# Optimization experiments

Hardware: AMD Instinct MI355X
Metric: run time of the kernel (lower is better)

The kernel has to match this reference:

```python
import jax, jax.numpy as jnp
import numpy as np

# Grid constants from voxel_size=(0.2,0.2,4), point_cloud_range=(0,-40,-3,70.4,40,1)
VX, VY, VZ = 0.2, 0.2, 4.0
PCR = (0.0, -40.0, -3.0, 70.4, 40.0, 1.0)
NX, NY, NZ = 352, 400, 1   # round((hi-lo)/v) per axis
BATCH = 2
N_POINTS = 400000
CANVAS = BATCH * NZ * NY * NX  # dense canvas of all voxels (segment ids)
EPS = 1e-3  # BN1d eps from norm_cfg


def _vidx(coors):
    # linear voxel index: b*Z*Y*X + z*Y*X + y*X + x  (coors = [b,z,y,x])
    c = coors.astype(jnp.int32)
    return ((c[:, 0] * NZ + c[:, 1]) * NY + c[:, 2]) * NX + c[:, 3]


def _seg_mean(x, idx):
    # scatter-mean over voxels (DynamicScatter, average_points=True)
    s = jax.ops.segment_sum(x, idx, num_segments=CANVAS)
    c = jax.ops.segment_sum(jnp.ones((x.shape[0], 1), x.dtype), idx, num_segments=CANVAS)
    return s / jnp.maximum(c, 1.0)


def _seg_max(x, idx):
    # scatter-max over voxels (DynamicScatter, average_points=False); empty voxels -> 0
    m = jax.ops.segment_max(x, idx, num_segments=CANVAS)
    c = jax.ops.segment_sum(jnp.ones((x.shape[0],), x.dtype), idx, num_segments=CANVAS)
    return jnp.where((c > 0)[:, None], m, jnp.zeros_like(m))


def _bn_relu(x, g, b):
    # BN1d in training mode (batch stats, biased var), affine, then ReLU
    mu = x.mean(axis=0)
    var = x.var(axis=0)
    return jax.nn.relu((x - mu) * jax.lax.rsqrt(var + EPS) * g + b)


def setup_inputs() -> dict:
    key = jax.random.key(0)
    ks = jax.random.split(key, 6)
    features = jax.random.normal(ks[0], (N_POINTS, 4), jnp.float32)
    # coors [b, z, y, x]; batch column sorted so coors[-1,0]+1 == batch_size
    half = N_POINTS // 2
    b = jnp.concatenate([jnp.zeros(half, jnp.int32), jnp.ones(N_POINTS - half, jnp.int32)])
    z = jnp.zeros(N_POINTS, jnp.int32)  # NZ == 1
    y = jax.random.randint(ks[1], (N_POINTS,), 0, NY, jnp.int32)
    x = jax.random.randint(ks[2], (N_POINTS,), 0, NX, jnp.int32)
    coors = jnp.stack([b, z, y, x], axis=1)
    # VFE params: layer0 Linear(10->64, no bias), layer1 Linear(128->128, no bias)
    W0 = jax.random.normal(ks[3], (10, 64), jnp.float32) * 0.1
    g0 = jnp.ones((64,), jnp.float32)
    b0 = jnp.zeros((64,), jnp.float32)
    W1 = jax.random.normal(ks[4], (128, 128), jnp.float32) * 0.1
    g1 = jnp.ones((128,), jnp.float32)
    b1 = jnp.zeros((128,), jnp.float32)
    return {"features": features, "coors": coors, "W0": W0, "g0": g0, "b0": b0,
            "W1": W1, "g1": g1, "b1": b1}


def reference(features, coors, W0, g0, b0, W1, g1, b1):
    idx = _vidx(coors)
    # cluster center: scatter-mean of point features, gather back to points
    vmean = _seg_mean(features, idx)
    pts_mean = vmean[idx]
    f_cluster = features[:, :3] - pts_mean[:, :3]
    # voxel center offset
    cf = coors.astype(features.dtype)
    f_center = jnp.stack([
        features[:, 0] - (cf[:, 3] * VX + (VX / 2 + PCR[0])),
        features[:, 1] - (cf[:, 2] * VY + (VY / 2 + PCR[1])),
        features[:, 2] - (cf[:, 1] * VZ + (VZ / 2 + PCR[2])),
    ], axis=1)
    feat = jnp.concatenate([features, f_cluster, f_center], axis=1)  # (N, 10)
    # VFE layer 0 + voxel max pool + gather-broadcast + concat
    pf0 = _bn_relu(feat @ W0, g0, b0)           # (N, 64)
    v0 = _seg_max(pf0, idx)                     # (CANVAS, 64)
    feat1 = jnp.concatenate([pf0, v0[idx]], axis=1)  # (N, 128)
    # VFE layer 1 + final voxel max pool
    pf1 = _bn_relu(feat1 @ W1, g1, b1)          # (N, 128)
    voxel_feats = _seg_max(pf1, idx)            # (CANVAS, 128), dense canvas
    return voxel_feats
```

## Files before the change

kernel.cpp:

```cpp
#include <hip/hip_runtime.h>

#define NPTS 400000
#define NXv 352
#define NYv 400
#define CANVAS 281600
#define NBLK2 6250
#define SCANB 275

typedef unsigned int uint;
typedef unsigned short ushort;
typedef __attribute__((ext_vector_type(8))) short short8;
typedef __attribute__((ext_vector_type(4))) float floatx4;

__device__ inline uint packbf(float a, float b) {
    uint ua = __float_as_uint(a);
    ua = (ua + 0x7fffu + ((ua >> 16) & 1u)) >> 16;
    uint ub = __float_as_uint(b);
    ub = (ub + 0x7fffu + ((ub >> 16) & 1u)) & 0xffff0000u;
    return ua | ub;
}
__device__ inline ushort bf16bits(float a) {
    uint u = __float_as_uint(a);
    return (ushort)((u + 0x7fffu + ((u >> 16) & 1u)) >> 16);
}
__device__ inline float lo16(uint u) { return __uint_as_float(u << 16); }
__device__ inline float hi16(uint u) { return __uint_as_float(u & 0xffff0000u); }
__device__ inline float bfval(ushort u) { return __uint_as_float(((uint)u) << 16); }

__global__ void k_bucket(const int4* __restrict__ coors, int* __restrict__ idxbuf,
                         int* __restrict__ pidx, uint* __restrict__ ucnt) {
    int i = blockIdx.x * 256 + threadIdx.x;
    if (i >= NPTS) return;
    int4 c = coors[i];
    int idx = ((c.x + c.y) * NYv + c.z) * NXv + c.w;
    idxbuf[i] = idx;
    pidx[i] = (int)atomicAdd(&ucnt[idx], 1u);
}

__global__ __launch_bounds__(1024) void k_scanA(const uint* __restrict__ ucnt,
                                                uint* __restrict__ voff,
                                                uint* __restrict__ bsum) {
    __shared__ uint sh[1024];
    int t = threadIdx.x;
    int v = blockIdx.x * 1024 + t;
    uint val = ucnt[v];
    sh[t] = val;
    for (int off = 1; off < 1024; off <<= 1) {
        __syncthreads();
        uint x = (t >= off) ? sh[t - off] : 0u;
        __syncthreads();
        sh[t] += x;
    }
    uint incl = sh[t];
    voff[v] = incl - val;
    if (t == 1023) bsum[blockIdx.x] = incl;
}

__global__ __launch_bounds__(1024) void k_scanC(const uint* __restrict__ bsum,
                                                uint* __restrict__ voff) {
    __shared__ uint sh[1024];
    __shared__ uint bs[1024];
    int t = threadIdx.x;
    uint val = (t < SCANB) ? bsum[t] : 0u;
    sh[t] = val; bs[t] = val;
    for (int off = 1; off < 1024; off <<= 1) {
        __syncthreads();
        uint x = (t >= off) ? sh[t - off] : 0u;
        __syncthreads();
        sh[t] += x;
    }
    __syncthreads();
    uint off_ = sh[blockIdx.x] - bs[blockIdx.x];
    int v = blockIdx.x * 1024 + t;
    voff[v] += off_;
    if (blockIdx.x == SCANB - 1 && t == 1023) voff[CANVAS] = NPTS;
}

__global__ void k_perm(const int* __restrict__ idxbuf, const int* __restrict__ pidx,
                       const uint* __restrict__ voff, int* __restrict__ perm,
                       int* __restrict__ vidx) {
    int i = blockIdx.x * 256 + threadIdx.x;
    if (i >= NPTS) return;
    int idx = idxbuf[i];
    uint j = voff[idx] + (uint)pidx[i];
    perm[j] = i;
    vidx[j] = idx;
}

__global__ void k_vmean(const float4* __restrict__ feat, const uint* __restrict__ voff,
                        const int* __restrict__ perm, float4* __restrict__ vmean) {
    int v = blockIdx.x * 256 + threadIdx.x;
    if (v >= CANVAS) return;
    uint s_ = voff[v], e_ = voff[v + 1];
    float4 s = make_float4(0.f, 0.f, 0.f, 0.f);
    for (uint j = s_; j < e_; ++j) {
        float4 f = feat[perm[j]];
        s.x += f.x; s.y += f.y; s.z += f.z; s.w += f.w;
    }
    float inv = 1.0f / (float)max((int)(e_ - s_), 1);
    vmean[v] = make_float4(s.x * inv, s.y * inv, s.z * inv, s.w * inv);
}

__global__ void k_prepw(const float* __restrict__ W1, ushort* __restrict__ w1t) {
    int i = blockIdx.x * 256 + threadIdx.x;
    if (i >= 16384) return;
    int n = i & 127, k = i >> 7;
    w1t[n * 128 + k] = bf16bits(W1[k * 128 + n]);
}

__global__ __launch_bounds__(256) void k_gemm1(
        const float4* __restrict__ feat, const int4* __restrict__ coors,
        const int* __restrict__ perm, const int* __restrict__ vidx,
        const float4* __restrict__ vmean, const float* __restrict__ W0,
        uint* __restrict__ x0u, float* __restrict__ stats) {
    __shared__ float w0s[640];
    __shared__ __align__(8) ushort tile[256 * 68];
    __shared__ float ps[128], qs[128];
    for (int t = threadIdx.x; t < 640; t += 256) w0s[t] = W0[t];
    __syncthreads();
    int j = blockIdx.x * 256 + threadIdx.x;
    bool valid = j < NPTS;
    ushort* trow = &tile[threadIdx.x * 68];
    if (valid) {
        int i = perm[j];
        float4 f = feat[i];
        int4 c = coors[i];
        float4 vm = vmean[vidx[j]];
        float ft[10];
        ft[0] = f.x; ft[1] = f.y; ft[2] = f.z; ft[3] = f.w;
        ft[4] = f.x - vm.x;
        ft[5] = f.y - vm.y;
        ft[6] = f.z - vm.z;
        ft[7] = f.x - ((float)c.w * 0.2f + 0.1f);
        ft[8] = f.y - ((float)c.z * 0.2f + (0.1f - 40.0f));
        ft[9] = f.z - ((float)c.y * 4.0f + (2.0f - 3.0f));
        uint* o = x0u + (size_t)j * 32;
        #pragma unroll
        for (int g = 0; g < 8; ++g) {
            float a[8];
            #pragma unroll
            for (int q = 0; q < 8; ++q) a[q] = 0.f;
            #pragma unroll
            for (int k = 0; k < 10; ++k) {
                float fk = ft[k];
                #pragma unroll
                for (int q = 0; q < 8; ++q) a[q] = fmaf(fk, w0s[k * 64 + g * 8 + q], a[q]);
            }
            uint4 w;
            w.x = packbf(a[0], a[1]); w.y = packbf(a[2], a[3]);
            w.z = packbf(a[4], a[5]); w.w = packbf(a[6], a[7]);
            *(uint4*)(o + g * 4) = w;
            ((uint2*)trow)[g * 2 + 0] = make_uint2(w.x, w.y);
            ((uint2*)trow)[g * 2 + 1] = make_uint2(w.z, w.w);
        }
    } else {
        #pragma unroll
        for (int g = 0; g < 16; ++g) ((uint2*)trow)[g] = make_uint2(0u, 0u);
    }
    __syncthreads();
    if (threadIdx.x < 128) {
        int c = threadIdx.x & 63, half = threadIdx.x >> 6;
        float s = 0.f, q = 0.f;
        for (int r = half * 128; r < half * 128 + 128; ++r) {
            float xv = bfval(tile[r * 68 + c]);
            s += xv;
            q = fmaf(xv, xv, q);
        }
        ps[half * 64 + c] = s;
        qs[half * 64 + c] = q;
    }
    __syncthreads();
    if (threadIdx.x < 64) {
        int c = threadIdx.x;
        atomicAdd(&stats[c], ps[c] + ps[64 + c]);
        atomicAdd(&stats[64 + c], qs[c] + qs[64 + c]);
    }
}

__global__ void k_bnfin(const float* __restrict__ sums, const float* __restrict__ g,
                        const float* __restrict__ b, float* __restrict__ ss, int C,
                        float invN) {
    int j = threadIdx.x;
    if (j >= C) return;
    float mu = sums[j] * invN;
    float var = sums[C + j] * invN - mu * mu;
    float istd = 1.0f / sqrtf(var + 1e-3f);
    float scale = istd * g[j];
    ss[j] = scale;
    ss[C + j] = b[j] - mu * scale;
}

__global__ void k_vmax0(const uint* __restrict__ x0u, const uint* __restrict__ voff,
                        const float* __restrict__ ss, uint* __restrict__ v0u) {
    __shared__ float s[128];
    if (threadIdx.x < 128) s[threadIdx.x] = ss[threadIdx.x];
    __syncthreads();
    int t = blockIdx.x * 256 + threadIdx.x;
    int v = t >> 4;
    if (v >= CANVAS) return;
    int c = (t & 15) << 2;
    uint s_ = voff[v], e_ = voff[v + 1];
    float4 m = make_float4(0.f, 0.f, 0.f, 0.f);
    for (uint j = s_; j < e_; ++j) {
        uint2 u = *(const uint2*)(x0u + (size_t)j * 32 + (c >> 1));
        m.x = fmaxf(m.x, fmaf(lo16(u.x), s[c + 0], s[64 + c + 0]));
        m.y = fmaxf(m.y, fmaf(hi16(u.x), s[c + 1], s[64 + c + 1]));
        m.z = fmaxf(m.z, fmaf(lo16(u.y), s[c + 2], s[64 + c + 2]));
        m.w = fmaxf(m.w, fmaf(hi16(u.y), s[c + 3], s[64 + c + 3]));
    }
    uint2 o; o.x = packbf(m.x, m.y); o.y = packbf(m.z, m.w);
    *(uint2*)(v0u + (size_t)v * 32 + (c >> 1)) = o;
}

__global__ __launch_bounds__(256) void k_gemm2m(
        const uint* __restrict__ x0u, const uint* __restrict__ v0u,
        const int* __restrict__ vidx, const float* __restrict__ ss,
        const ushort* __restrict__ w1t, uint* __restrict__ x1u,
        float* __restrict__ partial) {
    __shared__ __align__(16) ushort Bs[128 * 136];
    __shared__ __align__(16) ushort As[64 * 136];
    __shared__ float pst[4096];
    __shared__ float s[128];
    __shared__ int idxs[64];

    int r0 = blockIdx.x * 64;
    for (int i = threadIdx.x; i < 2048; i += 256) {
        int r = i >> 4, ch = i & 15;
        *(uint4*)&Bs[r * 136 + ch * 8] = *(const uint4*)&w1t[r * 128 + ch * 8];
    }
    if (threadIdx.x < 128) s[threadIdx.x] = ss[threadIdx.x];
    if (threadIdx.x < 64) idxs[threadIdx.x] = vidx[r0 + threadIdx.x];
    __syncthreads();

    for (int i = threadIdx.x; i < 512; i += 256) {
        int r = i >> 3, ch = i & 7, cb = ch * 8;
        uint4 u = *(const uint4*)(x0u + (size_t)(r0 + r) * 32 + ch * 4);
        uint w[4] = {u.x, u.y, u.z, u.w}, o[4];
        #pragma unroll
        for (int q2 = 0; q2 < 4; ++q2) {
            float a = fmaxf(fmaf(lo16(w[q2]), s[cb + 2 * q2], s[64 + cb + 2 * q2]), 0.f);
            float b = fmaxf(fmaf(hi16(w[q2]), s[cb + 2 * q2 + 1], s[64 + cb + 2 * q2 + 1]), 0.f);
            o[q2] = packbf(a, b);
        }
        *(uint4*)&As[r * 136 + ch * 8] = make_uint4(o[0], o[1], o[2], o[3]);
    }
    for (int i = threadIdx.x; i < 512; i += 256) {
        int r = i >> 3, ch = i & 7;
        *(uint4*)&As[r * 136 + 64 + ch * 8] =
            *(const uint4*)(v0u + (size_t)idxs[r] * 32 + ch * 4);
    }
    __syncthreads();

    int lane = threadIdx.x & 63, wid = threadIdx.x >> 6;
    int m = lane & 15, q = lane >> 4;
    const ushort* ar = &As[(wid * 16 + m) * 136 + q * 8];
    short8 a0 = *(const short8*)&ar[0];
    short8 a1 = *(const short8*)&ar[32];
    short8 a2 = *(const short8*)&ar[64];
    short8 a3 = *(const short8*)&ar[96];
    __syncthreads();

    #pragma unroll
    for (int ct = 0; ct < 8; ++ct) {
        const ushort* br = &Bs[(ct * 16 + m) * 136 + q * 8];
        short8 b0 = *(const short8*)&br[0];
        short8 b1 = *(const short8*)&br[32];
        short8 b2 = *(const short8*)&br[64];
        short8 b3 = *(const short8*)&br[96];
        floatx4 acc = {0.f, 0.f, 0.f, 0.f};
        acc = __builtin_amdgcn_mfma_f32_16x16x32_bf16(a0, b0, acc, 0, 0, 0);
        acc = __builtin_amdgcn_mfma_f32_16x16x32_bf16(a1, b1, acc, 0, 0, 0);
        acc = __builtin_amdgcn_mfma_f32_16x16x32_bf16(a2, b2, acc, 0, 0, 0);
        acc = __builtin_amdgcn_mfma_f32_16x16x32_bf16(a3, b3, acc, 0, 0, 0);
        float psv = acc[0] + acc[1] + acc[2] + acc[3];
        float pq = acc[0] * acc[0];
        pq = fmaf(acc[1], acc[1], pq);
        pq = fmaf(acc[2], acc[2], pq);
        pq = fmaf(acc[3], acc[3], pq);
        int col = ct * 16 + m;
        pst[(wid * 4 + q) * 128 + col] = psv;
        pst[2048 + (wid * 4 + q) * 128 + col] = pq;
        #pragma unroll
        for (int rg = 0; rg < 4; ++rg)
            As[(wid * 16 + q * 4 + rg) * 136 + ct * 16 + m] = bf16bits(acc[rg]);
    }
    __syncthreads();

    for (int i = threadIdx.x; i < 1024; i += 256) {
        int r = i >> 4, ch = i & 15;
        *(uint4*)(x1u + (size_t)(r0 + r) * 64 + ch * 4) = *(const uint4*)&As[r * 136 + ch * 8];
    }
    {
        int t = threadIdx.x;
        int base = (t < 128) ? 0 : 2048;
        int c = t & 127;
        float acc = 0.f;
        #pragma unroll
        for (int k = 0; k < 16; ++k) acc += pst[base + k * 128 + c];
        partial[(size_t)blockIdx.x * 256 + t] = acc;
    }
}

__global__ void k_red(const float* __restrict__ partial, float* __restrict__ sums) {
    int c = threadIdx.x;
    float s = 0.f;
    for (int r = blockIdx.x; r < NBLK2; r += gridDim.x) s += partial[(size_t)r * 256 + c];
    atomicAdd(&sums[c], s);
}

__global__ void k_vmax1(const uint2* __restrict__ x1u, const uint* __restrict__ voff,
                        const float* __restrict__ ss, float4* __restrict__ out) {
    __shared__ float s[256];
    s[threadIdx.x] = ss[threadIdx.x];
    __syncthreads();
    int t = blockIdx.x * 256 + threadIdx.x;
    int v = t >> 5;
    if (v >= CANVAS) return;
    int c = (t & 31) << 2;
    uint s_ = voff[v], e_ = voff[v + 1];
    float4 m = make_float4(0.f, 0.f, 0.f, 0.f);
    for (uint j = s_; j < e_; ++j) {
        uint2 u = x1u[(size_t)j * 32 + (c >> 2)];
        m.x = fmaxf(m.x, fmaf(lo16(u.x), s[c + 0], s[128 + c + 0]));
        m.y = fmaxf(m.y, fmaf(hi16(u.x), s[c + 1], s[128 + c + 1]));
        m.z = fmaxf(m.z, fmaf(lo16(u.y), s[c + 2], s[128 + c + 2]));
        m.w = fmaxf(m.w, fmaf(hi16(u.y), s[c + 3], s[128 + c + 3]));
    }
    out[(size_t)v * 32 + (c >> 2)] = m;
}

extern "C" void kernel_launch(void* const* d_in, const int* in_sizes, int n_in,
                              void* d_out, int out_size, void* d_ws, size_t ws_size,
                              hipStream_t stream) {
    const float4* feat  = (const float4*)d_in[0];
    const int4*   coors = (const int4*)d_in[1];
    const float*  W0    = (const float*)d_in[2];
    const float*  g0    = (const float*)d_in[3];
    const float*  b0    = (const float*)d_in[4];
    const float*  W1    = (const float*)d_in[5];
    const float*  g1    = (const float*)d_in[6];
    const float*  b1    = (const float*)d_in[7];

    char* ws = (char*)d_ws;
    int*    idxbuf = (int*)(ws + 0);
    int*    pidx   = (int*)(ws + 1600000);
    uint*   ucnt   = (uint*)(ws + 3200000);
    uint*   voff   = (uint*)(ws + 4326400);
    uint*   bsum   = (uint*)(ws + 5452816);
    float*  stats  = (float*)(ws + 5453936);
    int*    perm   = (int*)(ws + 5457008);
    int*    vidx   = (int*)(ws + 7057008);
    float*  vmean  = (float*)(ws + 8657008);
    ushort* w1t    = (ushort*)(ws + 13162608);
    uint*   x0u    = (uint*)(ws + 13195376);
    uint*   v0u    = (uint*)(ws + 64395376);
    uint*   x1u    = (uint*)(ws + 100440176);
    float*  part   = (float*)(ws + 202840176);

    hipMemsetAsync(ucnt, 0, 1126400, stream);
    hipMemsetAsync(stats, 0, 384 * sizeof(float), stream);

    const int BLK = 256;
    int gpts = (NPTS + BLK - 1) / BLK;
    int gvox = (CANVAS + BLK - 1) / BLK;

    k_bucket<<<gpts, BLK, 0, stream>>>(coors, idxbuf, pidx, ucnt);
    k_prepw<<<64, BLK, 0, stream>>>(W1, w1t);
    k_scanA<<<SCANB, 1024, 0, stream>>>(ucnt, voff, bsum);
    k_scanC<<<SCANB, 1024, 0, stream>>>(bsum, voff);
    k_perm<<<gpts, BLK, 0, stream>>>(idxbuf, pidx, voff, perm, vidx);
    k_vmean<<<gvox, BLK, 0, stream>>>(feat, voff, perm, (float4*)vmean);
    k_gemm1<<<gpts, BLK, 0, stream>>>(feat, coors, perm, vidx, (const float4*)vmean,
                                      W0, x0u, stats);
    k_bnfin<<<1, 64, 0, stream>>>(stats, g0, b0, stats + 384, 64, 1.0f / NPTS);
    k_vmax0<<<CANVAS * 16 / BLK, BLK, 0, stream>>>(x0u, voff, stats + 384, v0u);
    k_gemm2m<<<NBLK2, BLK, 0, stream>>>(x0u, v0u, vidx, stats + 384, w1t, x1u, part);
    k_red<<<64, BLK, 0, stream>>>(part, stats + 128);
    k_bnfin<<<1, 128, 0, stream>>>(stats + 128, g1, b1, stats + 512, 128, 1.0f / NPTS);
    k_vmax1<<<CANVAS * 32 / BLK, BLK, 0, stream>>>((const uint2*)x1u, voff,
                                                   stats + 512, (float4*)d_out);
}
```

Measured before the change: 453.8 us.

## Sort features during permutation, persist gemm2 with in-kernel BN stats, fuse small kernels

```diff
diff --git a/kernel.cpp b/kernel.cpp
--- a/kernel.cpp
+++ b/kernel.cpp
@@ -5,6 +5,7 @@
 #define NYv 400
 #define CANVAS 281600
 #define NBLK2 6250
+#define G2B 512
 #define SCANB 275
 
 typedef unsigned int uint;
@@ -27,14 +28,22 @@
 __device__ inline float hi16(uint u) { return __uint_as_float(u & 0xffff0000u); }
 __device__ inline float bfval(ushort u) { return __uint_as_float(((uint)u) << 16); }
 
-__global__ void k_bucket(const int4* __restrict__ coors, int* __restrict__ idxbuf,
-                         int* __restrict__ pidx, uint* __restrict__ ucnt) {
-    int i = blockIdx.x * 256 + threadIdx.x;
-    if (i >= NPTS) return;
-    int4 c = coors[i];
-    int idx = ((c.x + c.y) * NYv + c.z) * NXv + c.w;
-    idxbuf[i] = idx;
-    pidx[i] = (int)atomicAdd(&ucnt[idx], 1u);
+__global__ void k_bucket(const int4* __restrict__ coors, const float* __restrict__ W1,
+                         int* __restrict__ idxbuf, int* __restrict__ pidx,
+                         uint* __restrict__ ucnt, ushort* __restrict__ w1t) {
+    int b = blockIdx.x;
+    if (b < 1563) {
+        int i = b * 256 + threadIdx.x;
+        if (i >= NPTS) return;
+        int4 c = coors[i];
+        int idx = ((c.x + c.y) * NYv + c.z) * NXv + c.w;
+        idxbuf[i] = idx;
+        pidx[i] = (int)atomicAdd(&ucnt[idx], 1u);
+    } else {
+        int i = (b - 1563) * 256 + threadIdx.x;
+        int n = i & 127, k = i >> 7;
+        w1t[n * 128 + k] = bf16bits(W1[k * 128 + n]);
+    }
 }
 
 __global__ __launch_bounds__(1024) void k_scanA(const uint* __restrict__ ucnt,
@@ -77,40 +86,32 @@
 }
 
 __global__ void k_perm(const int* __restrict__ idxbuf, const int* __restrict__ pidx,
-                       const uint* __restrict__ voff, int* __restrict__ perm,
-                       int* __restrict__ vidx) {
+                       const uint* __restrict__ voff, const float4* __restrict__ feat,
+                       int* __restrict__ vidx, float4* __restrict__ featS) {
     int i = blockIdx.x * 256 + threadIdx.x;
     if (i >= NPTS) return;
     int idx = idxbuf[i];
     uint j = voff[idx] + (uint)pidx[i];
-    perm[j] = i;
     vidx[j] = idx;
-}
-
-__global__ void k_vmean(const float4* __restrict__ feat, const uint* __restrict__ voff,
-                        const int* __restrict__ perm, float4* __restrict__ vmean) {
+    featS[j] = feat[i];
+}
+
+__global__ void k_vmean(const float4* __restrict__ featS, const uint* __restrict__ voff,
+                        float4* __restrict__ vmean) {
     int v = blockIdx.x * 256 + threadIdx.x;
     if (v >= CANVAS) return;
     uint s_ = voff[v], e_ = voff[v + 1];
     float4 s = make_float4(0.f, 0.f, 0.f, 0.f);
     for (uint j = s_; j < e_; ++j) {
-        float4 f = feat[perm[j]];
+        float4 f = featS[j];
         s.x += f.x; s.y += f.y; s.z += f.z; s.w += f.w;
     }
     float inv = 1.0f / (float)max((int)(e_ - s_), 1);
     vmean[v] = make_float4(s.x * inv, s.y * inv, s.z * inv, s.w * inv);
 }
 
-__global__ void k_prepw(const float* __restrict__ W1, ushort* __restrict__ w1t) {
-    int i = blockIdx.x * 256 + threadIdx.x;
-    if (i >= 16384) return;
-    int n = i & 127, k = i >> 7;
-    w1t[n * 128 + k] = bf16bits(W1[k * 128 + n]);
-}
-
 __global__ __launch_bounds__(256) void k_gemm1(
-        const float4* __restrict__ feat, const int4* __restrict__ coors,
-        const int* __restrict__ perm, const int* __restrict__ vidx,
+        const float4* __restrict__ featS, const int* __restrict__ vidx,
         const float4* __restrict__ vmean, const float* __restrict__ W0,
         uint* __restrict__ x0u, float* __restrict__ stats) {
     __shared__ float w0s[640];
@@ -122,18 +123,19 @@
     bool valid = j < NPTS;
     ushort* trow = &tile[threadIdx.x * 68];
     if (valid) {
-        int i = perm[j];
-        float4 f = feat[i];
-        int4 c = coors[i];
-        float4 vm = vmean[vidx[j]];
+        float4 f = featS[j];
+        int idx = vidx[j];
+        float4 vm = vmean[idx];
+        int xq = idx % NXv;
+        int yq = (idx / NXv) % NYv;
         float ft[10];
         ft[0] = f.x; ft[1] = f.y; ft[2] = f.z; ft[3] = f.w;
         ft[4] = f.x - vm.x;
         ft[5] = f.y - vm.y;
         ft[6] = f.z - vm.z;
-        ft[7] = f.x - ((float)c.w * 0.2f + 0.1f);
-        ft[8] = f.y - ((float)c.z * 0.2f + (0.1f - 40.0f));
-        ft[9] = f.z - ((float)c.y * 4.0f + (2.0f - 3.0f));
+        ft[7] = f.x - ((float)xq * 0.2f + 0.1f);
+        ft[8] = f.y - ((float)yq * 0.2f - 39.9f);
+        ft[9] = f.z + 1.0f;
         uint* o = x0u + (size_t)j * 32;
         #pragma unroll
         for (int g = 0; g < 8; ++g) {
@@ -212,100 +214,110 @@
     *(uint2*)(v0u + (size_t)v * 32 + (c >> 1)) = o;
 }
 
-__global__ __launch_bounds__(256) void k_gemm2m(
+__global__ __launch_bounds__(256) void k_gemm2p(
         const uint* __restrict__ x0u, const uint* __restrict__ v0u,
         const int* __restrict__ vidx, const float* __restrict__ ss,
         const ushort* __restrict__ w1t, uint* __restrict__ x1u,
-        float* __restrict__ partial) {
+        float* __restrict__ sums) {
     __shared__ __align__(16) ushort Bs[128 * 136];
     __shared__ __align__(16) ushort As[64 * 136];
-    __shared__ float pst[4096];
+    __shared__ __align__(16) ushort Cs[64 * 136];
     __shared__ float s[128];
-    __shared__ int idxs[64];
-
-    int r0 = blockIdx.x * 64;
+
     for (int i = threadIdx.x; i < 2048; i += 256) {
         int r = i >> 4, ch = i & 15;
         *(uint4*)&Bs[r * 136 + ch * 8] = *(const uint4*)&w1t[r * 128 + ch * 8];
     }
     if (threadIdx.x < 128) s[threadIdx.x] = ss[threadIdx.x];
-    if (threadIdx.x < 64) idxs[threadIdx.x] = vidx[r0 + threadIdx.x];
-    __syncthreads();
-
-    for (int i = threadIdx.x; i < 512; i += 256) {
-        int r = i >> 3, ch = i & 7, cb = ch * 8;
-        uint4 u = *(const uint4*)(x0u + (size_t)(r0 + r) * 32 + ch * 4);
-        uint w[4] = {u.x, u.y, u.z, u.w}, o[4];
-        #pragma unroll
-        for (int q2 = 0; q2 < 4; ++q2) {
-            float a = fmaxf(fmaf(lo16(w[q2]), s[cb + 2 * q2], s[64 + cb + 2 * q2]), 0.f);
-            float b = fmaxf(fmaf(hi16(w[q2]), s[cb + 2 * q2 + 1], s[64 + cb + 2 * q2 + 1]), 0.f);
-            o[q2] = packbf(a, b);
-        }
-        *(uint4*)&As[r * 136 + ch * 8] = make_uint4(o[0], o[1], o[2], o[3]);
-    }
-    for (int i = threadIdx.x; i < 512; i += 256) {
-        int r = i >> 3, ch = i & 7;
-        *(uint4*)&As[r * 136 + 64 + ch * 8] =
-            *(const uint4*)(v0u + (size_t)idxs[r] * 32 + ch * 4);
-    }
-    __syncthreads();
 
     int lane = threadIdx.x & 63, wid = threadIdx.x >> 6;
     int m = lane & 15, q = lane >> 4;
-    const ushort* ar = &As[(wid * 16 + m) * 136 + q * 8];
-    short8 a0 = *(const short8*)&ar[0];
-    short8 a1 = *(const short8*)&ar[32];
-    short8 a2 = *(const short8*)&ar[64];
-    short8 a3 = *(const short8*)&ar[96];
-    __syncthreads();
-
+    int cch = threadIdx.x & 15;
+    float csum[8], csq[8];
     #pragma unroll
-    for (int ct = 0; ct < 8; ++ct) {
-        const ushort* br = &Bs[(ct * 16 + m) * 136 + q * 8];
-        short8 b0 = *(const short8*)&br[0];
-        short8 b1 = *(const short8*)&br[32];
-        short8 b2 = *(const short8*)&br[64];
-        short8 b3 = *(const short8*)&br[96];
-        floatx4 acc = {0.f, 0.f, 0.f, 0.f};
-        acc = __builtin_amdgcn_mfma_f32_16x16x32_bf16(a0, b0, acc, 0, 0, 0);
-        acc = __builtin_amdgcn_mfma_f32_16x16x32_bf16(a1, b1, acc, 0, 0, 0);
-        acc = __builtin_amdgcn_mfma_f32_16x16x32_bf16(a2, b2, acc, 0, 0, 0);
-        acc = __builtin_amdgcn_mfma_f32_16x16x32_bf16(a3, b3, acc, 0, 0, 0);
-        float psv = acc[0] + acc[1] + acc[2] + acc[3];
-        float pq = acc[0] * acc[0];
-        pq = fmaf(acc[1], acc[1], pq);
-        pq = fmaf(acc[2], acc[2], pq);
-        pq = fmaf(acc[3], acc[3], pq);
-        int col = ct * 16 + m;
-        pst[(wid * 4 + q) * 128 + col] = psv;
-        pst[2048 + (wid * 4 + q) * 128 + col] = pq;
-        #pragma unroll
-        for (int rg = 0; rg < 4; ++rg)
-            As[(wid * 16 + q * 4 + rg) * 136 + ct * 16 + m] = bf16bits(acc[rg]);
-    }
-    __syncthreads();
-
-    for (int i = threadIdx.x; i < 1024; i += 256) {
-        int r = i >> 4, ch = i & 15;
-        *(uint4*)(x1u + (size_t)(r0 + r) * 64 + ch * 4) = *(const uint4*)&As[r * 136 + ch * 8];
-    }
-    {
-        int t = threadIdx.x;
-        int base = (t < 128) ? 0 : 2048;
-        int c = t & 127;
-        float acc = 0.f;
-        #pragma unroll
-        for (int k = 0; k < 16; ++k) acc += pst[base + k * 128 + c];
-        partial[(size_t)blockIdx.x * 256 + t] = acc;
-    }
-}
-
-__global__ void k_red(const float* __restrict__ partial, float* __restrict__ sums) {
-    int c = threadIdx.x;
-    float s = 0.f;
-    for (int r = blockIdx.x; r < NBLK2; r += gridDim.x) s += partial[(size_t)r * 256 + c];
-    atomicAdd(&sums[c], s);
+    for (int k = 0; k < 8; ++k) { csum[k] = 0.f; csq[k] = 0.f; }
+    __syncthreads();
+
+    for (int st = blockIdx.x; st < NBLK2; st += G2B) {
+        int r0 = st * 64;
+        for (int i = threadIdx.x; i < 512; i += 256) {
+            int r = i >> 3, ch = i & 7, cb = ch * 8;
+            uint4 u = *(const uint4*)(x0u + (size_t)(r0 + r) * 32 + ch * 4);
+            uint w[4] = {u.x, u.y, u.z, u.w}, o[4];
+            #pragma unroll
+            for (int q2 = 0; q2 < 4; ++q2) {
+                float a = fmaxf(fmaf(lo16(w[q2]), s[cb + 2 * q2], s[64 + cb + 2 * q2]), 0.f);
+                float b = fmaxf(fmaf(hi16(w[q2]), s[cb + 2 * q2 + 1], s[64 + cb + 2 * q2 + 1]), 0.f);
+                o[q2] = packbf(a, b);
+            }
+            *(uint4*)&As[r * 136 + ch * 8] = make_uint4(o[0], o[1], o[2], o[3]);
+        }
+        for (int i = threadIdx.x; i < 512; i += 256) {
+            int r = i >> 3, ch = i & 7;
+            int vv = vidx[r0 + r];
+            *(uint4*)&As[r * 136 + 64 + ch * 8] = *(const uint4*)(v0u + (size_t)vv * 32 + ch * 4);
+        }
+        __syncthreads();
+
+        const ushort* ar = &As[(wid * 16 + m) * 136 + q * 8];
+        short8 a0 = *(const short8*)&ar[0];
+        short8 a1 = *(const short8*)&ar[32];
+        short8 a2 = *(const short8*)&ar[64];
+        short8 a3 = *(const short8*)&ar[96];
+        #pragma unroll
+        for (int ct = 0; ct < 8; ++ct) {
+            const ushort* br = &Bs[(ct * 16 + m) * 136 + q * 8];
+            short8 b0 = *(const short8*)&br[0];
+            short8 b1 = *(const short8*)&br[32];
+            short8 b2 = *(const short8*)&br[64];
+            short8 b3 = *(const short8*)&br[96];
+            floatx4 acc = {0.f, 0.f, 0.f, 0.f};
+            acc = __builtin_amdgcn_mfma_f32_16x16x32_bf16(a0, b0, acc, 0, 0, 0);
+            acc = __builtin_amdgcn_mfma_f32_16x16x32_bf16(a1, b1, acc, 0, 0, 0);
+            acc = __builtin_amdgcn_mfma_f32_16x16x32_bf16(a2, b2, acc, 0, 0, 0);
+            acc = __builtin_amdgcn_mfma_f32_16x16x32_bf16(a3, b3, acc, 0, 0, 0);
+            #pragma unroll
+            for (int rg = 0; rg < 4; ++rg)
+                Cs[(wid * 16 + q * 4 + rg) * 136 + ct * 16 + m] = bf16bits(acc[rg]);
+        }
+        __syncthreads();
+
+        for (int i = threadIdx.x; i < 1024; i += 256) {
+            int r = i >> 4;
+            uint4 cw = *(const uint4*)&Cs[r * 136 + cch * 8];
+            *(uint4*)(x1u + (size_t)(r0 + r) * 64 + cch * 4) = cw;
+            uint ww[4] = {cw.x, cw.y, cw.z, cw.w};
+            #pragma unroll
+            for (int k = 0; k < 4; ++k) {
+                float a = lo16(ww[k]), b = hi16(ww[k]);
+                csum[2 * k + 0] += a; csq[2 * k + 0] = fmaf(a, a, csq[2 * k + 0]);
+                csum[2 * k + 1] += b; csq[2 * k + 1] = fmaf(b, b, csq[2 * k + 1]);
+            }
+        }
+    }
+
+    __syncthreads();
+    float* red = (float*)As;
+    int g = threadIdx.x >> 4;
+    #pragma unroll
+    for (int k = 0; k < 8; ++k) red[g * 128 + cch * 8 + k] = csum[k];
+    __syncthreads();
+    if (threadIdx.x < 128) {
+        float tt = 0.f;
+        #pragma unroll
+        for (int k = 0; k < 16; ++k) tt += red[k * 128 + threadIdx.x];
+        atomicAdd(&sums[threadIdx.x], tt);
+    }
+    __syncthreads();
+    #pragma unroll
+    for (int k = 0; k < 8; ++k) red[g * 128 + cch * 8 + k] = csq[k];
+    __syncthreads();
+    if (threadIdx.x < 128) {
+        float tt = 0.f;
+        #pragma unroll
+        for (int k = 0; k < 16; ++k) tt += red[k * 128 + threadIdx.x];
+        atomicAdd(&sums[128 + threadIdx.x], tt);
+    }
 }
 
 __global__ void k_vmax1(const uint2* __restrict__ x1u, const uint* __restrict__ voff,
@@ -345,37 +357,33 @@
     int*    idxbuf = (int*)(ws + 0);
     int*    pidx   = (int*)(ws + 1600000);
     uint*   ucnt   = (uint*)(ws + 3200000);
-    uint*   voff   = (uint*)(ws + 4326400);
-    uint*   bsum   = (uint*)(ws + 5452816);
-    float*  stats  = (float*)(ws + 5453936);
-    int*    perm   = (int*)(ws + 5457008);
-    int*    vidx   = (int*)(ws + 7057008);
-    float*  vmean  = (float*)(ws + 8657008);
-    ushort* w1t    = (ushort*)(ws + 13162608);
-    uint*   x0u    = (uint*)(ws + 13195376);
-    uint*   v0u    = (uint*)(ws + 64395376);
-    uint*   x1u    = (uint*)(ws + 100440176);
-    float*  part   = (float*)(ws + 202840176);
-
-    hipMemsetAsync(ucnt, 0, 1126400, stream);
-    hipMemsetAsync(stats, 0, 384 * sizeof(float), stream);
+    float*  stats  = (float*)(ws + 4326400);
+    uint*   voff   = (uint*)(ws + 4329472);
+    uint*   bsum   = (uint*)(ws + 5455888);
+    int*    vidx   = (int*)(ws + 5459984);
+    float*  featS  = (float*)(ws + 7059984);
+    float*  vmean  = (float*)(ws + 13459984);
+    ushort* w1t    = (ushort*)(ws + 17965584);
+    uint*   x0u    = (uint*)(ws + 17998352);
+    uint*   v0u    = (uint*)(ws + 69198352);
+    uint*   x1u    = (uint*)(ws + 105243152);
+
+    hipMemsetAsync(ws + 3200000, 0, 1129472, stream);
 
     const int BLK = 256;
     int gpts = (NPTS + BLK - 1) / BLK;
     int gvox = (CANVAS + BLK - 1) / BLK;
 
-    k_bucket<<<gpts, BLK, 0, stream>>>(coors, idxbuf, pidx, ucnt);
-    k_prepw<<<64, BLK, 0, stream>>>(W1, w1t);
+    k_bucket<<<gpts + 64, BLK, 0, stream>>>(coors, W1, idxbuf, pidx, ucnt, w1t);
     k_scanA<<<SCANB, 1024, 0, stream>>>(ucnt, voff, bsum);
     k_scanC<<<SCANB, 1024, 0, stream>>>(bsum, voff);
-    k_perm<<<gpts, BLK, 0, stream>>>(idxbuf, pidx, voff, perm, vidx);
-    k_vmean<<<gvox, BLK, 0, stream>>>(feat, voff, perm, (float4*)vmean);
-    k_gemm1<<<gpts, BLK, 0, stream>>>(feat, coors, perm, vidx, (const float4*)vmean,
+    k_perm<<<gpts, BLK, 0, stream>>>(idxbuf, pidx, voff, feat, vidx, (float4*)featS);
+    k_vmean<<<gvox, BLK, 0, stream>>>((const float4*)featS, voff, (float4*)vmean);
+    k_gemm1<<<gpts, BLK, 0, stream>>>((const float4*)featS, vidx, (const float4*)vmean,
                                       W0, x0u, stats);
     k_bnfin<<<1, 64, 0, stream>>>(stats, g0, b0, stats + 384, 64, 1.0f / NPTS);
     k_vmax0<<<CANVAS * 16 / BLK, BLK, 0, stream>>>(x0u, voff, stats + 384, v0u);
-    k_gemm2m<<<NBLK2, BLK, 0, stream>>>(x0u, v0u, vidx, stats + 384, w1t, x1u, part);
-    k_red<<<64, BLK, 0, stream>>>(part, stats + 128);
+    k_gemm2p<<<G2B, BLK, 0, stream>>>(x0u, v0u, vidx, stats + 384, w1t, x1u, stats + 128);
     k_bnfin<<<1, 128, 0, stream>>>(stats + 128, g1, b1, stats + 512, 128, 1.0f / NPTS);
     k_vmax1<<<CANVAS * 32 / BLK, BLK, 0, stream>>>((const uint2*)x1u, voff,
                                                    stats + 512, (float4*)d_out);
```

New measurement: 397.2 us. -12.5%, faster.
